# Optimization experiments

Hardware: AMD Instinct MI355X
Metric: run time of the kernel (lower is better)

## Reference

```python
import jax, jax.numpy as jnp
import numpy as np

N_NODES = 100000
N_EDGES = 1600000
HID = 64


def _gcn_conv(x, src, dst, W, b, n_nodes):
    """PyG GCNConv: add self-loops, symmetric deg normalization, linear transform.
    out_i = sum_{j in N(i) u {i}} deg_i^{-1/2} deg_j^{-1/2} (x_j W) + b
    """
    h = x @ W  # [N, out] small matmul
    loops = jnp.arange(n_nodes, dtype=src.dtype)
    s = jnp.concatenate([src, loops])  # sources (message senders)
    d = jnp.concatenate([dst, loops])  # targets (aggregation index)
    deg = jax.ops.segment_sum(jnp.ones_like(d, dtype=h.dtype), d, num_segments=n_nodes)
    dinv = jnp.where(deg > 0, jax.lax.rsqrt(deg), 0.0)
    coef = dinv[s] * dinv[d]  # [E+N]
    msg = h[s] * coef[:, None]  # gather + scale (memory-bound)
    out = jax.ops.segment_sum(msg, d, num_segments=n_nodes)  # scatter-add
    return out + b


def setup_inputs() -> dict:
    key = jax.random.key(0)
    ks = jax.random.split(key, 16)
    x = jax.random.normal(ks[0], (N_NODES, 4), dtype=jnp.float32)
    edge_index = jax.random.randint(ks[1], (2, N_EDGES), 0, N_NODES, dtype=jnp.int64)
    s = 0.1
    params = {
        'W1': jax.random.normal(ks[2], (4, HID), dtype=jnp.float32) * s,
        'b1': jnp.zeros((HID,), dtype=jnp.float32),
        'W2': jax.random.normal(ks[3], (HID, HID), dtype=jnp.float32) * s,
        'b2': jnp.zeros((HID,), dtype=jnp.float32),
        'W3': jax.random.normal(ks[4], (HID, HID), dtype=jnp.float32) * s,
        'b3': jnp.zeros((HID,), dtype=jnp.float32),
        'Wp': jax.random.normal(ks[5], (HID, HID), dtype=jnp.float32) * s,
        'bp': jnp.zeros((HID,), dtype=jnp.float32),
        'Wa': jax.random.normal(ks[6], (HID, 4), dtype=jnp.float32) * s,
        'ba': jnp.zeros((4,), dtype=jnp.float32),
        'Wm': jax.random.normal(ks[7], (HID, 2), dtype=jnp.float32) * s,
        'bm': jnp.zeros((2,), dtype=jnp.float32),
        'Wg': jax.random.normal(ks[8], (HID, 3), dtype=jnp.float32) * s,
        'bg': jnp.zeros((3,), dtype=jnp.float32),
        'Wt': jax.random.normal(ks[9], (HID, 10), dtype=jnp.float32) * s,
        'bt': jnp.zeros((10,), dtype=jnp.float32),
    }
    return {'x': x, 'edge_index': edge_index, 'node_index': 0, **params}


def reference(x, edge_index, node_index, W1, b1, W2, b2, W3, b3, Wp, bp, Wa, ba, Wm, bm, Wg, bg, Wt, bt):
    src, dst = edge_index[0], edge_index[1]
    n = x.shape[0]
    # dropout is identity in eval mode
    h = jax.nn.relu(_gcn_conv(x, src, dst, W1, b1, n))
    h = jax.nn.relu(_gcn_conv(h, src, dst, W2, b2, n))
    h = jax.nn.relu(_gcn_conv(h, src, dst, W3, b3, n))
    node = h[node_index]
    node = jax.nn.relu(node @ Wp + bp)
    return (node @ Wa + ba, node @ Wm + bm, node @ Wg + bg, node @ Wt + bt)
```

## Files before the change

### kernel.cpp

```cpp
#include <hip/hip_runtime.h>


#define HID  64
#define CAP1 2048
#define CAP2 512
#define RB1  128
#define RB2  128
#define CL3  2048
#define VE   8
#define TPB  256
#define TT   1024
#define NW   16

__device__ __forceinline__ int detect64(const void* ei) {
  const unsigned* e32 = (const unsigned*)ei;
  int lane = threadIdx.x & 63;
  bool z = (e32[2 * lane + 1] == 0u);
  return (__ballot(z) == ~0ull) ? 1 : 0;
}

__device__ __forceinline__ int ld_src(const void* ei, int is64, long long e) {
  return is64 ? (int)((const unsigned*)ei)[e << 1] : ((const int*)ei)[e];
}

__device__ __forceinline__ int load_dsts(const void* ei, long long E, long long base,
                                         int is64, int d[VE]) {
  int n = (int)((E - base) < VE ? (E - base) : VE);
  if (is64) {
    const unsigned long long* p = (const unsigned long long*)ei + E + base;
    if (n == VE && (((E + base) & 1) == 0)) {
      const ulonglong2* q = (const ulonglong2*)p;
#pragma unroll
      for (int k = 0; k < VE / 2; ++k) {
        ulonglong2 v = q[k];
        d[2 * k] = (int)(unsigned)v.x; d[2 * k + 1] = (int)(unsigned)v.y;
      }
    } else {
      for (int k = 0; k < n; ++k) d[k] = (int)(unsigned)p[k];
    }
  } else {
    const int* p = (const int*)ei + E + base;
    if (n == VE && (((E + base) & 3) == 0)) {
      const int4* q = (const int4*)p;
#pragma unroll
      for (int k = 0; k < VE / 4; ++k) {
        int4 v = q[k];
        d[4 * k] = v.x; d[4 * k + 1] = v.y; d[4 * k + 2] = v.z; d[4 * k + 3] = v.w;
      }
    } else {
      for (int k = 0; k < n; ++k) d[k] = p[k];
    }
  }
  return n;
}

__device__ __forceinline__ int load_dsts32(const int* dst32, long long E,
                                           long long base, int d[VE]) {
  int n = (int)((E - base) < VE ? (E - base) : VE);
  if (n == VE) {
    int4 a = ((const int4*)(dst32 + base))[0];
    int4 b = ((const int4*)(dst32 + base))[1];
    d[0] = a.x; d[1] = a.y; d[2] = a.z; d[3] = a.w;
    d[4] = b.x; d[5] = b.y; d[6] = b.z; d[7] = b.w;
  } else {
    for (int k = 0; k < n; ++k) d[k] = dst32[base + k];
  }
  return n;
}

__global__ void k_scanF1(const void* ei, int E, const int* nidx_p, int* dst32,
                         int* slot2, int* node2, int* cnt2, int* l3, int* ec3) {
  int is64 = detect64(ei);
  int nidx = *nidx_p;
  if (blockIdx.x == 0 && threadIdx.x == 0) {
    if (atomicCAS(&slot2[nidx], 0, -1) == 0) {
      int p = atomicAdd(cnt2, 1) & (CAP2 - 1);
      slot2[nidx] = p + 1; node2[p] = nidx;
    }
  }
  long long base = ((long long)blockIdx.x * TPB + threadIdx.x) * VE;
  if (base >= E) return;
  int d[VE];
  int n = load_dsts(ei, E, base, is64, d);
  if (n == VE) {
    ((int4*)(dst32 + base))[0] = make_int4(d[0], d[1], d[2], d[3]);
    ((int4*)(dst32 + base))[1] = make_int4(d[4], d[5], d[6], d[7]);
  } else {
    for (int k = 0; k < n; ++k) dst32[base + k] = d[k];
  }
  for (int k = 0; k < n; ++k) {
    if (d[k] == nidx) {
      int s = ld_src(ei, is64, base + k);
      if (atomicCAS(&slot2[s], 0, -1) == 0) {
        int p = atomicAdd(cnt2, 1) & (CAP2 - 1);
        slot2[s] = p + 1; node2[p] = s;
      }
      int q = atomicAdd(ec3, 1);
      if (q < CL3) l3[q] = s;
    }
  }
}

__global__ void k_scanF2(const void* ei, int E, const int* dst32,
                         const int* slot2, const int* node2, const int* cnt2,
                         int* slot1, int* node1, int* need, int* cnt1,
                         int* rc2, int* bl2) {
  int rows2 = min(*cnt2, CAP2);
  for (int r = threadIdx.x; r < rows2; r += TPB) {
    int i = node2[r];
    need[i] = 1;
    if (atomicCAS(&slot1[i], 0, -1) == 0) {
      int p = atomicAdd(cnt1, 1) & (CAP1 - 1);
      slot1[i] = p + 1; node1[p] = i;
    }
  }
  int is64 = detect64(ei);
  long long base = ((long long)blockIdx.x * TPB + threadIdx.x) * VE;
  if (base >= E) return;
  int d[VE];
  int n = load_dsts32(dst32, E, base, d);
  for (int k = 0; k < n; ++k) {
    int sv = slot2[d[k]];
    if (sv > 0) {
      int ad = sv - 1;
      int s = ld_src(ei, is64, base + k);
      need[s] = 1;
      if (atomicCAS(&slot1[s], 0, -1) == 0) {
        int p = atomicAdd(cnt1, 1) & (CAP1 - 1);
        slot1[s] = p + 1; node1[p] = s;
      }
      int q = atomicAdd(&rc2[ad], 1);
      if (q < RB2) bl2[ad * RB2 + q] = s;
    }
  }
}

__global__ void k_scanS(const void* ei, int E, const int* dst32,
                        const int* slot1, int* need, int* rc1, int* bl1) {
  int is64 = detect64(ei);
  long long base = ((long long)blockIdx.x * TPB + threadIdx.x) * VE;
  if (base >= E) return;
  int d[VE];
  int n = load_dsts32(dst32, E, base, d);
  for (int k = 0; k < n; ++k) {
    int sv = slot1[d[k]];
    if (sv > 0) {
      int ad = sv - 1;
      int s = ld_src(ei, is64, base + k);
      need[s] = 1;
      int q = atomicAdd(&rc1[ad], 1);
      if (q < RB1) bl1[ad * RB1 + q] = s;
    }
  }
}

__global__ void k_scanDeg(int E, const int* dst32, const int* need, int* deg) {
  long long base = ((long long)blockIdx.x * TPB + threadIdx.x) * VE;
  if (base >= E) return;
  int d[VE];
  int n = load_dsts32(dst32, E, base, d);
  for (int k = 0; k < n; ++k)
    if (need[d[k]]) atomicAdd(&deg[d[k]], 1);
}

__global__ void k_l1(const float* __restrict__ x, const float* __restrict__ W1,
                     const float* __restrict__ b1, const int* __restrict__ deg,
                     const int* __restrict__ node1, const int* __restrict__ cnt1,
                     const int* __restrict__ rc1, const int* __restrict__ bl1,
                     float* __restrict__ h1c) {
  int w = blockIdx.x * 4 + (threadIdx.x >> 6);
  int lane = threadIdx.x & 63;
  int rows = min(*cnt1, CAP1);
  if (w >= rows) return;
  int i = node1[w];
  float di = 1.0f / sqrtf((float)(deg[i] + 1));
  int cnt = min(rc1[w], RB1);
  float ax = 0.f, ay = 0.f, az = 0.f, aw = 0.f;
  for (int j = lane; j < cnt; j += 64) {
    int s = bl1[w * RB1 + j];
    float c = (1.0f / sqrtf((float)(deg[s] + 1))) * di;
    float4 xv = ((const float4*)x)[s];
    ax += c * xv.x; ay += c * xv.y; az += c * xv.z; aw += c * xv.w;
  }
#pragma unroll
  for (int t = 1; t < 64; t <<= 1) {
    ax += __shfl_xor(ax, t); ay += __shfl_xor(ay, t);
    az += __shfl_xor(az, t); aw += __shfl_xor(aw, t);
  }
  float4 xi = ((const float4*)x)[i];
  float dd = di * di;
  ax += dd * xi.x; ay += dd * xi.y; az += dd * xi.z; aw += dd * xi.w;
  float v = ax * W1[lane] + ay * W1[64 + lane] + az * W1[128 + lane] +
            aw * W1[192 + lane] + b1[lane];
  h1c[w * HID + lane] = v > 0.f ? v : 0.f;
}

__global__ __launch_bounds__(TT) void k_l2tail(
    const float* __restrict__ W2, const float* __restrict__ b2,
    const int* __restrict__ deg, const int* __restrict__ node2,
    const int* __restrict__ cnt2, const int* __restrict__ slot1,
    const int* __restrict__ rc2, const int* __restrict__ bl2,
    const float* __restrict__ h1c, float* __restrict__ h2c,
    const int* __restrict__ nidx_p, const int* __restrict__ slot2,
    const int* __restrict__ l3, const int* __restrict__ ec3,
    const float* __restrict__ W3, const float* __restrict__ b3,
    const float* __restrict__ Wp, const float* __restrict__ bp,
    const float* __restrict__ Wa, const float* __restrict__ ba,
    const float* __restrict__ Wm, const float* __restrict__ bm,
    const float* __restrict__ Wg, const float* __restrict__ bg,
    const float* __restrict__ Wt, const float* __restrict__ bt,
    float* __restrict__ out) {
  __shared__ float h2s[64][HID];
  __shared__ float sh[NW][HID];
  __shared__ float part[NW][HID];
  __shared__ float g3[HID];
  __shared__ float h3[HID];
  __shared__ float p[HID];
  __shared__ int   ssl[64];
  __shared__ float scc[64];
  int tid = threadIdx.x, wv = tid >> 6, lane = tid & 63;
  int nidx = *nidx_p;
  int rows = min(*cnt2, CAP2);

  for (int w = wv; w < rows; w += NW) {
    int i = node2[w];
    float di = 1.0f / sqrtf((float)(deg[i] + 1));
    int cnt = min(rc2[w], RB2);
    float acc = 0.f;
    for (int j0 = 0; j0 < cnt; j0 += 64) {
      int nb = min(64, cnt - j0);
      int sl = 0; float c = 0.f;
      if (lane < nb) {
        int s = bl2[w * RB2 + j0 + lane];
        sl = slot1[s] - 1;
        c = (1.0f / sqrtf((float)(deg[s] + 1))) * di;
      }
      int j = 0;
      for (; j + 8 <= nb; j += 8) {
        int r0 = __shfl(sl, j + 0), r1 = __shfl(sl, j + 1);
        int r2 = __shfl(sl, j + 2), r3 = __shfl(sl, j + 3);
        int r4 = __shfl(sl, j + 4), r5 = __shfl(sl, j + 5);
        int r6 = __shfl(sl, j + 6), r7 = __shfl(sl, j + 7);
        float v0 = h1c[r0 * HID + lane];
        float v1 = h1c[r1 * HID + lane];
        float v2 = h1c[r2 * HID + lane];
        float v3 = h1c[r3 * HID + lane];
        float v4 = h1c[r4 * HID + lane];
        float v5 = h1c[r5 * HID + lane];
        float v6 = h1c[r6 * HID + lane];
        float v7 = h1c[r7 * HID + lane];
        acc += __shfl(c, j + 0) * v0 + __shfl(c, j + 1) * v1 +
               __shfl(c, j + 2) * v2 + __shfl(c, j + 3) * v3 +
               __shfl(c, j + 4) * v4 + __shfl(c, j + 5) * v5 +
               __shfl(c, j + 6) * v6 + __shfl(c, j + 7) * v7;
      }
      for (; j < nb; ++j)
        acc += __shfl(c, j) * h1c[__shfl(sl, j) * HID + lane];
    }
    acc += di * di * h1c[(slot1[i] - 1) * HID + lane];
    sh[wv][lane] = acc;
    float v = b2[lane];
#pragma unroll 16
    for (int k = 0; k < HID; ++k) v += sh[wv][k] * W2[k * HID + lane];
    v = v > 0.f ? v : 0.f;
    if (w < 64) h2s[w][lane] = v; else h2c[w * HID + lane] = v;
  }
  __syncthreads();

  float dn = 1.0f / sqrtf((float)(deg[nidx] + 1));
  int cnt = min(*ec3, CL3);
  float acc = 0.f;
  for (int j0 = 0; j0 < cnt; j0 += 64) {
    int nb = min(64, cnt - j0);
    if (tid < nb) {
      int s = l3[j0 + tid];
      ssl[tid] = slot2[s] - 1;
      scc[tid] = (1.0f / sqrtf((float)(deg[s] + 1))) * dn;
    }
    __syncthreads();
    int j = wv;
    for (; j + 48 < nb; j += 64) {
      int r0 = ssl[j], r1 = ssl[j + 16], r2 = ssl[j + 32], r3 = ssl[j + 48];
      float v0 = (r0 < 64) ? h2s[r0][lane] : h2c[r0 * HID + lane];
      float v1 = (r1 < 64) ? h2s[r1][lane] : h2c[r1 * HID + lane];
      float v2 = (r2 < 64) ? h2s[r2][lane] : h2c[r2 * HID + lane];
      float v3 = (r3 < 64) ? h2s[r3][lane] : h2c[r3 * HID + lane];
      acc += scc[j] * v0 + scc[j + 16] * v1 + scc[j + 32] * v2 +
             scc[j + 48] * v3;
    }
    for (; j < nb; j += NW) {
      int r = ssl[j];
      float hv = (r < 64) ? h2s[r][lane] : h2c[r * HID + lane];
      acc += scc[j] * hv;
    }
    __syncthreads();
  }
  part[wv][lane] = acc;
  __syncthreads();
  if (wv == 0) {
    float a = 0.f;
#pragma unroll
    for (int u = 0; u < NW; ++u) a += part[u][lane];
    int r = slot2[nidx] - 1;
    float hv = (r < 64) ? h2s[r][lane] : h2c[r * HID + lane];
    g3[lane] = a + dn * dn * hv;
  }
  __syncthreads();
  {
    int k0 = wv * 4;
    float v = g3[k0] * W3[k0 * HID + lane] +
              g3[k0 + 1] * W3[(k0 + 1) * HID + lane] +
              g3[k0 + 2] * W3[(k0 + 2) * HID + lane] +
              g3[k0 + 3] * W3[(k0 + 3) * HID + lane];
    part[wv][lane] = v;
  }
  __syncthreads();
  if (wv == 0) {
    float v = b3[lane];
#pragma unroll
    for (int u = 0; u < NW; ++u) v += part[u][lane];
    h3[lane] = v > 0.f ? v : 0.f;
  }
  __syncthreads();
  {
    int k0 = wv * 4;
    float v = h3[k0] * Wp[k0 * HID + lane] +
              h3[k0 + 1] * Wp[(k0 + 1) * HID + lane] +
              h3[k0 + 2] * Wp[(k0 + 2) * HID + lane] +
              h3[k0 + 3] * Wp[(k0 + 3) * HID + lane];
    part[wv][lane] = v;
  }
  __syncthreads();
  if (wv == 0) {
    float v = bp[lane];
#pragma unroll
    for (int u = 0; u < NW; ++u) v += part[u][lane];
    p[lane] = v > 0.f ? v : 0.f;
  }
  __syncthreads();
  if (tid < 4) {
    float o = ba[tid];
#pragma unroll 8
    for (int k = 0; k < HID; ++k) o += p[k] * Wa[k * 4 + tid];
    out[tid] = o;
  } else if (tid < 6) {
    int c = tid - 4; float o = bm[c];
#pragma unroll 8
    for (int k = 0; k < HID; ++k) o += p[k] * Wm[k * 2 + c];
    out[tid] = o;
  } else if (tid < 9) {
    int c = tid - 6; float o = bg[c];
#pragma unroll 8
    for (int k = 0; k < HID; ++k) o += p[k] * Wg[k * 3 + c];
    out[tid] = o;
  } else if (tid < 19) {
    int c = tid - 9; float o = bt[c];
#pragma unroll 8
    for (int k = 0; k < HID; ++k) o += p[k] * Wt[k * 10 + c];
    out[tid] = o;
  }
}

extern "C" void kernel_launch(void* const* d_in, const int* in_sizes, int n_in,
                              void* d_out, int out_size, void* d_ws, size_t ws_size,
                              hipStream_t stream) {
  const float* x  = (const float*)d_in[0];
  const void*  ei = d_in[1];
  const int* nidx = (const int*)d_in[2];
  const float* W1 = (const float*)d_in[3];
  const float* b1 = (const float*)d_in[4];
  const float* W2 = (const float*)d_in[5];
  const float* b2 = (const float*)d_in[6];
  const float* W3 = (const float*)d_in[7];
  const float* b3 = (const float*)d_in[8];
  const float* Wp = (const float*)d_in[9];
  const float* bp = (const float*)d_in[10];
  const float* Wa = (const float*)d_in[11];
  const float* ba = (const float*)d_in[12];
  const float* Wm = (const float*)d_in[13];
  const float* bm = (const float*)d_in[14];
  const float* Wg = (const float*)d_in[15];
  const float* bg = (const float*)d_in[16];
  const float* Wt = (const float*)d_in[17];
  const float* bt = (const float*)d_in[18];
  float* out = (float*)d_out;

  int N = in_sizes[0] / 4;
  int E = in_sizes[1] / 2;

  char* w = (char*)d_ws;
  size_t o = 0;
  auto take = [&](size_t bytes) -> void* {
    void* p = w + o;
    o += (bytes + 255) & ~(size_t)255;
    return p;
  };
  size_t zeroInts = (size_t)8 + 2 * (size_t)N + CAP1 + CAP2 + 2 * (size_t)N;
  int* zr = (int*)take(zeroInts * 4);
  int* cnt1  = zr + 0;
  int* cnt2  = zr + 1;
  int* ec3   = zr + 2;
  int* deg   = zr + 8;
  int* need  = deg + N;
  int* rc1   = need + N;
  int* rc2   = rc1 + CAP1;
  int* slot1 = rc2 + CAP2;
  int* slot2 = slot1 + N;
  int*   dst32 = (int*)take((size_t)E * 4);
  int*   node1 = (int*)take((size_t)CAP1 * 4);
  int*   node2 = (int*)take((size_t)CAP2 * 4);
  int*   bl1   = (int*)take((size_t)CAP1 * RB1 * 4);
  int*   bl2   = (int*)take((size_t)CAP2 * RB2 * 4);
  int*   l3    = (int*)take((size_t)CL3 * 4);
  float* h1c   = (float*)take((size_t)CAP1 * HID * 4);
  float* h2c   = (float*)take((size_t)CAP2 * HID * 4);

  int gS = (int)(((long long)E + TPB * VE - 1) / (TPB * VE));

  hipMemsetAsync(zr, 0x00, zeroInts * 4, stream);
  k_scanF1 <<<gS, TPB, 0, stream>>>(ei, E, nidx, dst32, slot2, node2, cnt2, l3, ec3);
  k_scanF2 <<<gS, TPB, 0, stream>>>(ei, E, dst32, slot2, node2, cnt2,
                                    slot1, node1, need, cnt1, rc2, bl2);
  k_scanS  <<<gS, TPB, 0, stream>>>(ei, E, dst32, slot1, need, rc1, bl1);
  k_scanDeg<<<gS, TPB, 0, stream>>>(E, dst32, need, deg);
  k_l1     <<<CAP1 / 4, TPB, 0, stream>>>(x, W1, b1, deg, node1, cnt1, rc1, bl1, h1c);
  k_l2tail <<<1, TT, 0, stream>>>(W2, b2, deg, node2, cnt2, slot1, rc2, bl2,
                                  h1c, h2c, nidx, slot2, l3, ec3, W3, b3,
                                  Wp, bp, Wa, ba, Wm, bm, Wg, bg, Wt, bt, out);
}
```

Before: 169.2 us.

## Replace dense slot2/need membership arrays with bitmaps and move zeroing into scan

Replaces the per-node int arrays slot2 and need with small atomic bitmaps (bm2, bm1, bmN), so the random membership probes in the four edge scans touch a few KB that stay cache-resident instead of 400 KB arrays. The slot2 index lookup is replaced by linear searches over node2, and in the tail kernel over a shared-memory copy of node2. Zeroing of deg/slot1/rc arrays moves from hipMemsetAsync into the first scan kernel, leaving a much smaller memset. The linear searches add per-hit loops over up to a few hundred entries, and zeroing inside k_scanF1 is only safe if no thread reads those arrays before the kernel finishes.

```diff
diff --git a/kernel.cpp b/kernel.cpp
--- a/kernel.cpp
+++ b/kernel.cpp
@@ -11,6 +11,15 @@
 #define TPB  256
 #define TT   1024
 #define NW   16
+#define BMW  3200
+
+__device__ __forceinline__ int bmTest(const unsigned* bm, int i) {
+  return (bm[i >> 5] >> (i & 31)) & 1u;
+}
+__device__ __forceinline__ int bmSet(unsigned* bm, int i) {
+  unsigned old = atomicOr(&bm[i >> 5], 1u << (i & 31));
+  return !((old >> (i & 31)) & 1u);
+}
 
 __device__ __forceinline__ int detect64(const void* ei) {
   const unsigned* e32 = (const unsigned*)ei;
@@ -69,16 +78,20 @@
 }
 
 __global__ void k_scanF1(const void* ei, int E, const int* nidx_p, int* dst32,
-                         int* slot2, int* node2, int* cnt2, int* l3, int* ec3) {
+                         unsigned* bm2, int* node2, int* cnt2, int* l3, int* ec3,
+                         int4* zbig, int zi4) {
+  int gid = blockIdx.x * TPB + threadIdx.x;
+  for (int i = gid; i < zi4; i += gridDim.x * TPB)
+    zbig[i] = make_int4(0, 0, 0, 0);
   int is64 = detect64(ei);
   int nidx = *nidx_p;
-  if (blockIdx.x == 0 && threadIdx.x == 0) {
-    if (atomicCAS(&slot2[nidx], 0, -1) == 0) {
+  if (gid == 0) {
+    if (bmSet(bm2, nidx)) {
       int p = atomicAdd(cnt2, 1) & (CAP2 - 1);
-      slot2[nidx] = p + 1; node2[p] = nidx;
-    }
-  }
-  long long base = ((long long)blockIdx.x * TPB + threadIdx.x) * VE;
+      node2[p] = nidx;
+    }
+  }
+  long long base = (long long)gid * VE;
   if (base >= E) return;
   int d[VE];
   int n = load_dsts(ei, E, base, is64, d);
@@ -91,9 +104,9 @@
   for (int k = 0; k < n; ++k) {
     if (d[k] == nidx) {
       int s = ld_src(ei, is64, base + k);
-      if (atomicCAS(&slot2[s], 0, -1) == 0) {
+      if (bmSet(bm2, s)) {
         int p = atomicAdd(cnt2, 1) & (CAP2 - 1);
-        slot2[s] = p + 1; node2[p] = s;
+        node2[p] = s;
       }
       int q = atomicAdd(ec3, 1);
       if (q < CL3) l3[q] = s;
@@ -102,13 +115,15 @@
 }
 
 __global__ void k_scanF2(const void* ei, int E, const int* dst32,
-                         const int* slot2, const int* node2, const int* cnt2,
-                         int* slot1, int* node1, int* need, int* cnt1,
+                         const unsigned* bm2, const int* node2, const int* cnt2,
+                         unsigned* bm1, unsigned* bmN,
+                         int* slot1, int* node1, int* cnt1,
                          int* rc2, int* bl2) {
   int rows2 = min(*cnt2, CAP2);
   for (int r = threadIdx.x; r < rows2; r += TPB) {
     int i = node2[r];
-    need[i] = 1;
+    bmSet(bmN, i);
+    bmSet(bm1, i);
     if (atomicCAS(&slot1[i], 0, -1) == 0) {
       int p = atomicAdd(cnt1, 1) & (CAP1 - 1);
       slot1[i] = p + 1; node1[p] = i;
@@ -120,11 +135,13 @@
   int d[VE];
   int n = load_dsts32(dst32, E, base, d);
   for (int k = 0; k < n; ++k) {
-    int sv = slot2[d[k]];
-    if (sv > 0) {
-      int ad = sv - 1;
+    if (bmTest(bm2, d[k])) {
+      int ad = 0;
+      for (int r = 0; r < rows2; ++r)
+        if (node2[r] == d[k]) { ad = r; break; }
       int s = ld_src(ei, is64, base + k);
-      need[s] = 1;
+      bmSet(bmN, s);
+      bmSet(bm1, s);
       if (atomicCAS(&slot1[s], 0, -1) == 0) {
         int p = atomicAdd(cnt1, 1) & (CAP1 - 1);
         slot1[s] = p + 1; node1[p] = s;
@@ -136,31 +153,32 @@
 }
 
 __global__ void k_scanS(const void* ei, int E, const int* dst32,
-                        const int* slot1, int* need, int* rc1, int* bl1) {
+                        const unsigned* bm1, const int* slot1, unsigned* bmN,
+                        int* rc1, int* bl1) {
   int is64 = detect64(ei);
   long long base = ((long long)blockIdx.x * TPB + threadIdx.x) * VE;
   if (base >= E) return;
   int d[VE];
   int n = load_dsts32(dst32, E, base, d);
   for (int k = 0; k < n; ++k) {
-    int sv = slot1[d[k]];
-    if (sv > 0) {
-      int ad = sv - 1;
+    if (bmTest(bm1, d[k])) {
+      int ad = slot1[d[k]] - 1;
       int s = ld_src(ei, is64, base + k);
-      need[s] = 1;
+      bmSet(bmN, s);
       int q = atomicAdd(&rc1[ad], 1);
       if (q < RB1) bl1[ad * RB1 + q] = s;
     }
   }
 }
 
-__global__ void k_scanDeg(int E, const int* dst32, const int* need, int* deg) {
+__global__ void k_scanDeg(int E, const int* dst32, const unsigned* bmN,
+                          int* deg) {
   long long base = ((long long)blockIdx.x * TPB + threadIdx.x) * VE;
   if (base >= E) return;
   int d[VE];
   int n = load_dsts32(dst32, E, base, d);
   for (int k = 0; k < n; ++k)
-    if (need[d[k]]) atomicAdd(&deg[d[k]], 1);
+    if (bmTest(bmN, d[k])) atomicAdd(&deg[d[k]], 1);
 }
 
 __global__ void k_l1(const float* __restrict__ x, const float* __restrict__ W1,
@@ -201,7 +219,7 @@
     const int* __restrict__ cnt2, const int* __restrict__ slot1,
     const int* __restrict__ rc2, const int* __restrict__ bl2,
     const float* __restrict__ h1c, float* __restrict__ h2c,
-    const int* __restrict__ nidx_p, const int* __restrict__ slot2,
+    const int* __restrict__ nidx_p,
     const int* __restrict__ l3, const int* __restrict__ ec3,
     const float* __restrict__ W3, const float* __restrict__ b3,
     const float* __restrict__ Wp, const float* __restrict__ bp,
@@ -218,12 +236,15 @@
   __shared__ float p[HID];
   __shared__ int   ssl[64];
   __shared__ float scc[64];
+  __shared__ int   sn2[CAP2];
   int tid = threadIdx.x, wv = tid >> 6, lane = tid & 63;
   int nidx = *nidx_p;
   int rows = min(*cnt2, CAP2);
+  for (int r = tid; r < rows; r += TT) sn2[r] = node2[r];
+  __syncthreads();
 
   for (int w = wv; w < rows; w += NW) {
-    int i = node2[w];
+    int i = sn2[w];
     float di = 1.0f / sqrtf((float)(deg[i] + 1));
     int cnt = min(rc2[w], RB2);
     float acc = 0.f;
@@ -274,7 +295,10 @@
     int nb = min(64, cnt - j0);
     if (tid < nb) {
       int s = l3[j0 + tid];
-      ssl[tid] = slot2[s] - 1;
+      int r = 0;
+      for (int u = 0; u < rows; ++u)
+        if (sn2[u] == s) { r = u; break; }
+      ssl[tid] = r;
       scc[tid] = (1.0f / sqrtf((float)(deg[s] + 1))) * dn;
     }
     __syncthreads();
@@ -301,7 +325,9 @@
     float a = 0.f;
 #pragma unroll
     for (int u = 0; u < NW; ++u) a += part[u][lane];
-    int r = slot2[nidx] - 1;
+    int r = 0;
+    for (int u = 0; u < rows; ++u)
+      if (sn2[u] == nidx) { r = u; break; }
     float hv = (r < 64) ? h2s[r][lane] : h2c[r * HID + lane];
     g3[lane] = a + dn * dn * hv;
   }
@@ -395,17 +421,20 @@
     o += (bytes + 255) & ~(size_t)255;
     return p;
   };
-  size_t zeroInts = (size_t)8 + 2 * (size_t)N + CAP1 + CAP2 + 2 * (size_t)N;
+  size_t zeroInts = 16 + 3 * BMW;
   int* zr = (int*)take(zeroInts * 4);
-  int* cnt1  = zr + 0;
-  int* cnt2  = zr + 1;
-  int* ec3   = zr + 2;
-  int* deg   = zr + 8;
-  int* need  = deg + N;
-  int* rc1   = need + N;
+  int*      cnt1 = zr + 0;
+  int*      cnt2 = zr + 1;
+  int*      ec3  = zr + 2;
+  unsigned* bm2  = (unsigned*)(zr + 16);
+  unsigned* bm1  = bm2 + BMW;
+  unsigned* bmN  = bm1 + BMW;
+  int zbigInts = 2 * N + CAP1 + CAP2;
+  int* zbig  = (int*)take((size_t)zbigInts * 4);
+  int* deg   = zbig;
+  int* slot1 = deg + N;
+  int* rc1   = slot1 + N;
   int* rc2   = rc1 + CAP1;
-  int* slot1 = rc2 + CAP2;
-  int* slot2 = slot1 + N;
   int*   dst32 = (int*)take((size_t)E * 4);
   int*   node1 = (int*)take((size_t)CAP1 * 4);
   int*   node2 = (int*)take((size_t)CAP2 * 4);
@@ -416,15 +445,17 @@
   float* h2c   = (float*)take((size_t)CAP2 * HID * 4);
 
   int gS = (int)(((long long)E + TPB * VE - 1) / (TPB * VE));
+  int zi4 = zbigInts / 4;
 
   hipMemsetAsync(zr, 0x00, zeroInts * 4, stream);
-  k_scanF1 <<<gS, TPB, 0, stream>>>(ei, E, nidx, dst32, slot2, node2, cnt2, l3, ec3);
-  k_scanF2 <<<gS, TPB, 0, stream>>>(ei, E, dst32, slot2, node2, cnt2,
-                                    slot1, node1, need, cnt1, rc2, bl2);
-  k_scanS  <<<gS, TPB, 0, stream>>>(ei, E, dst32, slot1, need, rc1, bl1);
-  k_scanDeg<<<gS, TPB, 0, stream>>>(E, dst32, need, deg);
+  k_scanF1 <<<gS, TPB, 0, stream>>>(ei, E, nidx, dst32, bm2, node2, cnt2,
+                                    l3, ec3, (int4*)zbig, zi4);
+  k_scanF2 <<<gS, TPB, 0, stream>>>(ei, E, dst32, bm2, node2, cnt2,
+                                    bm1, bmN, slot1, node1, cnt1, rc2, bl2);
+  k_scanS  <<<gS, TPB, 0, stream>>>(ei, E, dst32, bm1, slot1, bmN, rc1, bl1);
+  k_scanDeg<<<gS, TPB, 0, stream>>>(E, dst32, bmN, deg);
   k_l1     <<<CAP1 / 4, TPB, 0, stream>>>(x, W1, b1, deg, node1, cnt1, rc1, bl1, h1c);
   k_l2tail <<<1, TT, 0, stream>>>(W2, b2, deg, node2, cnt2, slot1, rc2, bl2,
-                                  h1c, h2c, nidx, slot2, l3, ec3, W3, b3,
+                                  h1c, h2c, nidx, l3, ec3, W3, b3,
                                   Wp, bp, Wa, ba, Wm, bm, Wg, bg, Wt, bt, out);
 }
```

Measured after the change: 169.9 us. No clear change (+0.4%).
